# Optimization experiments

Hardware: AMD Instinct MI355X
Metric: run time of the kernel (lower is better)

The kernel has to match this reference:

```python
import jax, jax.numpy as jnp
import numpy as np

ENC_DIM = 128
DEC_DIM = 128
NUM_HEADS = 4
HEAD_DIM = DEC_DIM // NUM_HEADS


def _layernorm(x, g, b, eps=1e-5):
    mu = jnp.mean(x, axis=-1, keepdims=True)
    var = jnp.mean((x - mu) ** 2, axis=-1, keepdims=True)
    return (x - mu) * jax.lax.rsqrt(var + eps) * g + b


def setup_inputs() -> dict:
    key = jax.random.key(0)
    ks = jax.random.split(key, 12)
    B, H, W, D = 2, 16, 16, 16
    s = 0.02
    return {
        "encoder_feat": jax.random.normal(ks[0], (B, ENC_DIM, H, W, D), jnp.float32),
        "decoder_feat": jax.random.normal(ks[1], (B, DEC_DIM, H, W, D), jnp.float32),
        # torch Linear weights stored as [out, in]
        "Wq": jax.random.normal(ks[2], (DEC_DIM, DEC_DIM), jnp.float32) * s,
        "bq": jnp.zeros((DEC_DIM,), jnp.float32),
        "Wk": jax.random.normal(ks[3], (DEC_DIM, ENC_DIM), jnp.float32) * s,
        "bk": jnp.zeros((DEC_DIM,), jnp.float32),
        "Wv": jax.random.normal(ks[4], (DEC_DIM, ENC_DIM), jnp.float32) * s,
        "bv": jnp.zeros((DEC_DIM,), jnp.float32),
        "Wo": jax.random.normal(ks[5], (DEC_DIM, DEC_DIM), jnp.float32) * s,
        "bo": jnp.zeros((DEC_DIM,), jnp.float32),
        "g_enc": jnp.ones((ENC_DIM,), jnp.float32),
        "b_enc": jnp.zeros((ENC_DIM,), jnp.float32),
        "g_dec": jnp.ones((DEC_DIM,), jnp.float32),
        "b_dec": jnp.zeros((DEC_DIM,), jnp.float32),
        "g_out": jnp.ones((DEC_DIM,), jnp.float32),
        "b_out": jnp.zeros((DEC_DIM,), jnp.float32),
        "W1": jax.random.normal(ks[6], (DEC_DIM * 4, DEC_DIM), jnp.float32) * s,
        "b1": jnp.zeros((DEC_DIM * 4,), jnp.float32),
        "W2": jax.random.normal(ks[7], (DEC_DIM, DEC_DIM * 4), jnp.float32) * s,
        "b2": jnp.zeros((DEC_DIM,), jnp.float32),
    }


def reference(encoder_feat, decoder_feat, Wq, bq, Wk, bk, Wv, bv, Wo, bo,
              g_enc, b_enc, g_dec, b_dec, g_out, b_out, W1, b1, W2, b2):
    B, C_dec, H, W_, D = decoder_feat.shape
    N = H * W_ * D
    scale = HEAD_DIM ** -0.5
    # [B, C, H, W, D] -> [B, N, C]
    enc_seq = encoder_feat.reshape(B, -1, N).transpose(0, 2, 1)
    dec_seq = decoder_feat.reshape(B, C_dec, N).transpose(0, 2, 1)
    enc_seq = _layernorm(enc_seq, g_enc, b_enc)
    dec_seq = _layernorm(dec_seq, g_dec, b_dec)
    # projections (torch Linear: x @ W.T + b), split heads -> [B, h, N, d]
    Q = (dec_seq @ Wq.T + bq).reshape(B, N, NUM_HEADS, HEAD_DIM).transpose(0, 2, 1, 3)
    K = (enc_seq @ Wk.T + bk).reshape(B, N, NUM_HEADS, HEAD_DIM).transpose(0, 2, 1, 3)
    V = (enc_seq @ Wv.T + bv).reshape(B, N, NUM_HEADS, HEAD_DIM).transpose(0, 2, 1, 3)
    attn = jnp.einsum('bhqd,bhkd->bhqk', Q, K) * scale  # [B, h, N, N]
    attn = jax.nn.softmax(attn, axis=-1)
    out = jnp.einsum('bhqk,bhkd->bhqd', attn, V)
    out = out.transpose(0, 2, 1, 3).reshape(B, N, C_dec)
    out = out @ Wo.T + bo
    out = dec_seq + out
    h = _layernorm(out, g_out, b_out)
    ffn = jax.nn.gelu(h @ W1.T + b1, approximate=False) @ W2.T + b2
    out = out + ffn
    return out.transpose(0, 2, 1).reshape(B, C_dec, H, W_, D)
```

## Files before the change

### kernel.cpp

```cpp
#include <hip/hip_runtime.h>
#include <hip/hip_bf16.h>
#include <math.h>

#define B_ 2
#define N_ 4096
#define BN_ 8192
#define NH_ 4
#define SPLIT_ 8

using bf16x8   = __attribute__((ext_vector_type(8))) __bf16;
using f32x4    = __attribute__((ext_vector_type(4))) float;
using ushortx8 = __attribute__((ext_vector_type(8))) unsigned short;

#if __has_builtin(__builtin_amdgcn_exp2f)
#define FAST_EXP2(x) __builtin_amdgcn_exp2f(x)
#else
#define FAST_EXP2(x) __expf((x) * 0.6931471805599453f)
#endif

static __device__ __forceinline__ unsigned short f2bf(float f) {
    union { __hip_bfloat16 h; unsigned short u; } c;
    c.h = __float2bfloat16(f);
    return c.u;
}
static __device__ __forceinline__ float bf2f(unsigned short u) {
    union { __hip_bfloat16 h; unsigned short u; } c;
    c.u = u;
    return __bfloat162float(c.h);
}
static __device__ __forceinline__ unsigned int pk2bf(float lo, float hi) {
    return __builtin_amdgcn_perm(__float_as_uint(hi) + 0x8000u,
                                 __float_as_uint(lo) + 0x8000u, 0x07060302u);
}

__global__ __launch_bounds__(256)
void fused_pre_kernel(const float* __restrict__ Wq, const float* __restrict__ Wk,
                      const float* __restrict__ Wv, const float* __restrict__ Wo,
                      const float* __restrict__ W1, const float* __restrict__ W2,
                      unsigned short* __restrict__ wq, unsigned short* __restrict__ wk,
                      unsigned short* __restrict__ wv, unsigned short* __restrict__ wo,
                      unsigned short* __restrict__ w1, unsigned short* __restrict__ w2,
                      const float* __restrict__ enc, const float* __restrict__ dec,
                      const float* __restrict__ g_enc, const float* __restrict__ b_enc,
                      const float* __restrict__ g_dec, const float* __restrict__ b_dec,
                      unsigned short* __restrict__ enc_out,
                      unsigned short* __restrict__ dec_out) {
    __shared__ float tile[128][33];
    __shared__ float mu_s[32], inv_s[32];
    const int t = threadIdx.x;
    if (blockIdx.x < 768) {
        const int id = blockIdx.x * 256 + t;
        if      (id <  16384) wq[id]          = f2bf(Wq[id]);
        else if (id <  32768) wk[id - 16384]  = f2bf(Wk[id - 16384]);
        else if (id <  49152) wv[id - 32768]  = f2bf(Wv[id - 32768]);
        else if (id <  65536) wo[id - 49152]  = f2bf(Wo[id - 49152]);
        else if (id < 131072) w1[id - 65536]  = f2bf(W1[id - 65536]);
        else                  w2[id - 131072] = f2bf(W2[id - 131072]);
        return;
    }
    const int idx = blockIdx.x - 768;
    const int x = idx & 127;
    const int b = (idx >> 7) & 1;
    const int z = idx >> 8;
    const float* in     = z ? dec   : enc;
    const float* gamma  = z ? g_dec : g_enc;
    const float* beta   = z ? b_dec : b_enc;
    unsigned short* outb = z ? dec_out : enc_out;
    const int n0 = x * 32;
    const float* inb = in + (size_t)b * 128 * N_;

    {
        const int col = t & 31;
        const int r0  = t >> 5;
        for (int j = 0; j < 16; ++j) {
            const int r = r0 + 8 * j;
            tile[r][col] = inb[(size_t)r * N_ + n0 + col];
        }
    }
    __syncthreads();
    {
        const int tok = t >> 3;
        const int ln  = t & 7;
        float s = 0.f, ss = 0.f;
        for (int c = ln; c < 128; c += 8) {
            const float x2 = tile[c][tok];
            s += x2; ss += x2 * x2;
        }
        for (int m = 1; m < 8; m <<= 1) {
            s  += __shfl_xor(s, m);
            ss += __shfl_xor(ss, m);
        }
        if (ln == 0) {
            const float mu  = s * (1.f / 128.f);
            const float var = ss * (1.f / 128.f) - mu * mu;
            mu_s[tok]  = mu;
            inv_s[tok] = rsqrtf(var + 1e-5f);
        }
    }
    __syncthreads();
    const size_t obase = ((size_t)b * N_ + n0) * 128;
    for (int j = 0; j < 16; ++j) {
        const int f  = t + 256 * j;
        const int tk = f >> 7;
        const int c  = f & 127;
        const float x2 = tile[c][tk];
        outb[obase + f] = f2bf((x2 - mu_s[tk]) * inv_s[tk] * gamma[c] + beta[c]);
    }
}

__global__ __launch_bounds__(128)
void qkv_gemm_kernel(const unsigned short* __restrict__ decb,
                     const unsigned short* __restrict__ encb,
                     const unsigned short* __restrict__ wq,
                     const unsigned short* __restrict__ wk,
                     const unsigned short* __restrict__ wv,
                     const float* __restrict__ bq, const float* __restrict__ bk,
                     const float* __restrict__ bv,
                     unsigned short* __restrict__ Qh, unsigned short* __restrict__ Kh,
                     unsigned short* __restrict__ Vt) {
    const int z = blockIdx.y;
    const int t = threadIdx.x;
    const int wvx = t >> 6, lane = t & 63;
    const int l15 = lane & 15, quad = lane >> 4;
    const int m0 = blockIdx.x * 32 + wvx * 16;
    const unsigned short* X    = (z == 0) ? decb : encb;
    const unsigned short* Wb   = (z == 0) ? wq : (z == 1) ? wk : wv;
    const float*          bias = (z == 0) ? bq : (z == 1) ? bk : bv;

    bf16x8 af[4];
    #pragma unroll
    for (int kk = 0; kk < 4; ++kk)
        af[kk] = *(const bf16x8*)(X + (size_t)(m0 + l15) * 128 + kk * 32 + quad * 8);

    f32x4 acc[8];
    #pragma unroll
    for (int nb = 0; nb < 8; ++nb) {
        f32x4 a = {0.f, 0.f, 0.f, 0.f};
        #pragma unroll
        for (int kk = 0; kk < 4; ++kk) {
            const bf16x8 wf = *(const bf16x8*)(Wb + (size_t)(nb * 16 + l15) * 128 + kk * 32 + quad * 8);
            a = __builtin_amdgcn_mfma_f32_16x16x32_bf16(af[kk], wf, a, 0, 0, 0);
        }
        acc[nb] = a;
    }

    const float qsc = 0.17677669529663687f * 1.4426950408889634f;
    const int b   = m0 >> 12;
    const int nb0 = (m0 & 4095) + quad * 4;
    #pragma unroll
    for (int nb = 0; nb < 8; ++nb) {
        const int col = nb * 16 + l15;
        const int h = col >> 5, d = col & 31;
        const float bz = bias[col];
        if (z == 2) {
            ushort4 pk;
            pk.x = f2bf(acc[nb][0] + bz);
            pk.y = f2bf(acc[nb][1] + bz);
            pk.z = f2bf(acc[nb][2] + bz);
            pk.w = f2bf(acc[nb][3] + bz);
            *(ushort4*)(Vt + ((size_t)(b * NH_ + h) * 32 + d) * N_ + nb0) = pk;
        } else {
            unsigned short* dst = (z == 0) ? Qh : Kh;
            const float sc = (z == 0) ? qsc : 1.f;
            #pragma unroll
            for (int r = 0; r < 4; ++r) {
                const int n = nb0 + r;
                dst[((size_t)(b * NH_ + h) * N_ + n) * 32 + d] = f2bf((acc[nb][r] + bz) * sc);
            }
        }
    }
}

__global__ __launch_bounds__(256)
void attn_kernel5(const unsigned short* __restrict__ Qh,
                  const unsigned short* __restrict__ Kh,
                  const unsigned short* __restrict__ Vt,
                  unsigned short* __restrict__ Op,
                  unsigned short* __restrict__ lp) {
    __shared__ alignas(16) unsigned short sP[4][64][72];

    const int gid   = blockIdx.x;
    const int combo = gid & 63;
    const int qblk  = gid >> 6;
    const int bh    = combo & 7;
    const int s     = combo >> 3;
    const int t  = threadIdx.x;
    const int wvx = t >> 6, lane = t & 63;
    const int l15 = lane & 15, quad = lane >> 4;
    const int qw = qblk * 256 + wvx * 64;
    const size_t hbse = (size_t)bh * N_ * 32;

    bf16x8 qf[4];
    #pragma unroll
    for (int f = 0; f < 4; ++f)
        qf[f] = *(const bf16x8*)(Qh + hbse + (size_t)(qw + f * 16 + l15) * 32 + quad * 8);

    const unsigned short* Kp = Kh + hbse;
    const unsigned short* Vp = Vt + (size_t)bh * 32 * N_;

    f32x4 o0[4], o1[4];
    float l[4];
    #pragma unroll
    for (int f = 0; f < 4; ++f) {
        o0[f] = f32x4{0.f, 0.f, 0.f, 0.f};
        o1[f] = f32x4{0.f, 0.f, 0.f, 0.f};
        l[f] = 0.f;
    }
    const f32x4 zero = {0.f, 0.f, 0.f, 0.f};

    const int kbeg = s * (N_ / SPLIT_);
    const int kend = kbeg + (N_ / SPLIT_);

    bf16x8 kf[4];
    #pragma unroll
    for (int c = 0; c < 4; ++c)
        kf[c] = *(const bf16x8*)(Kp + (size_t)(kbeg + c * 16 + l15) * 32 + quad * 8);

    for (int k0 = kbeg; k0 < kend; k0 += 64) {
        bf16x8 va[2], vb[2];
        #pragma unroll
        for (int s2 = 0; s2 < 2; ++s2) {
            va[s2] = *(const bf16x8*)(Vp + (size_t)l15 * N_        + k0 + s2 * 32 + quad * 8);
            vb[s2] = *(const bf16x8*)(Vp + (size_t)(16 + l15) * N_ + k0 + s2 * 32 + quad * 8);
        }
        const int kn = (k0 + 64 < kend) ? (k0 + 64) : kbeg;
        bf16x8 kfn[4];
        #pragma unroll
        for (int c = 0; c < 4; ++c)
            kfn[c] = *(const bf16x8*)(Kp + (size_t)(kn + c * 16 + l15) * 32 + quad * 8);

        #pragma unroll
        for (int f = 0; f < 4; ++f) {
            #pragma unroll
            for (int c = 0; c < 4; ++c) {
                const f32x4 sv = __builtin_amdgcn_mfma_f32_16x16x32_bf16(kf[c], qf[f], zero, 0, 0, 0);
                const float p0 = FAST_EXP2(sv[0]);
                const float p1 = FAST_EXP2(sv[1]);
                const float p2 = FAST_EXP2(sv[2]);
                const float p3 = FAST_EXP2(sv[3]);
                l[f] += (p0 + p1) + (p2 + p3);
                uint2 pk;
                pk.x = pk2bf(p0, p1);
                pk.y = pk2bf(p2, p3);
                *(uint2*)&sP[wvx][f * 16 + l15][c * 16 + quad * 4] = pk;
            }
        }
        #pragma unroll
        for (int f = 0; f < 4; ++f) {
            #pragma unroll
            for (int s2 = 0; s2 < 2; ++s2) {
                const bf16x8 pf = *(const bf16x8*)&sP[wvx][f * 16 + l15][s2 * 32 + quad * 8];
                o0[f] = __builtin_amdgcn_mfma_f32_16x16x32_bf16(va[s2], pf, o0[f], 0, 0, 0);
                o1[f] = __builtin_amdgcn_mfma_f32_16x16x32_bf16(vb[s2], pf, o1[f], 0, 0, 0);
            }
        }
        #pragma unroll
        for (int c = 0; c < 4; ++c) kf[c] = kfn[c];
    }

    #pragma unroll
    for (int f = 0; f < 4; ++f) {
        float lf = l[f];
        lf += __shfl_xor(lf, 16);
        lf += __shfl_xor(lf, 32);
        const int tok = qw + f * 16 + l15;
        const size_t ob = ((size_t)(s * 8 + bh) * N_ + tok) * 32;
        uint2 w0, w1v;
        w0.x  = pk2bf(o0[f][0], o0[f][1]); w0.y  = pk2bf(o0[f][2], o0[f][3]);
        w1v.x = pk2bf(o1[f][0], o1[f][1]); w1v.y = pk2bf(o1[f][2], o1[f][3]);
        *(uint2*)&Op[ob + quad * 4]      = w0;
        *(uint2*)&Op[ob + 16 + quad * 4] = w1v;
        if (quad == 0)
            lp[(size_t)(s * 8 + bh) * N_ + tok] = f2bf(lf);
    }
}

__global__ __launch_bounds__(256)
void fused_tail2_kernel(const unsigned short* __restrict__ Op,
                        const unsigned short* __restrict__ lp,
                        const unsigned short* __restrict__ wo,
                        const float* __restrict__ bo,
                        const unsigned short* __restrict__ decb,
                        const float* __restrict__ g, const float* __restrict__ be,
                        const unsigned short* __restrict__ w1,
                        const float* __restrict__ b1,
                        const unsigned short* __restrict__ w2,
                        const float* __restrict__ b2,
                        float* __restrict__ out) {
    __shared__ alignas(16) float sred[4][64][32];
    __shared__ float sln[4][2][16];
    __shared__ alignas(16) unsigned short hb_lds[16][136];
    __shared__ alignas(16) unsigned short smid[16][536];
    const int t = threadIdx.x;
    const int wv = t >> 6, lane = t & 63;
    const int l15 = lane & 15, quad = lane >> 4;
    const int m0 = blockIdx.x * 16;

    const int tokA = m0 + l15;
    const int bA = tokA >> 12, nA = tokA & 4095;
    const int bhh = bA * NH_ + wv;
    bf16x8 af;
    {
        f32x4 sa = {0.f, 0.f, 0.f, 0.f}, sb = {0.f, 0.f, 0.f, 0.f};
        float lt = 0.f;
        #pragma unroll
        for (int s = 0; s < SPLIT_; ++s) {
            const size_t base = ((size_t)(s * 8 + bhh) * N_ + nA) * 32 + quad * 8;
            const ushortx8 u = *(const ushortx8*)&Op[base];
            sa[0] += bf2f(u[0]); sa[1] += bf2f(u[1]);
            sa[2] += bf2f(u[2]); sa[3] += bf2f(u[3]);
            sb[0] += bf2f(u[4]); sb[1] += bf2f(u[5]);
            sb[2] += bf2f(u[6]); sb[3] += bf2f(u[7]);
            lt += bf2f(lp[(size_t)(s * 8 + bhh) * N_ + nA]);
        }
        const float inv = 1.f / lt;
        union { uint4 u; bf16x8 v; } cvt;
        cvt.u.x = pk2bf(sa[0] * inv, sa[1] * inv);
        cvt.u.y = pk2bf(sa[2] * inv, sa[3] * inv);
        cvt.u.z = pk2bf(sb[0] * inv, sb[1] * inv);
        cvt.u.w = pk2bf(sb[2] * inv, sb[3] * inv);
        af = cvt.v;
    }

    #pragma unroll
    for (int nb = 0; nb < 8; ++nb) {
        const bf16x8 wf = *(const bf16x8*)(wo + (size_t)(nb * 16 + l15) * 128
                                           + wv * 32 + quad * 8);
        const f32x4 a = __builtin_amdgcn_mfma_f32_16x16x32_bf16(
            af, wf, f32x4{0.f, 0.f, 0.f, 0.f}, 0, 0, 0);
        *(f32x4*)&sred[wv][lane][nb * 4] = a;
    }
    __syncthreads();

    float v[2][4];
    #pragma unroll
    for (int lnb = 0; lnb < 2; ++lnb) {
        const int nbg = 2 * wv + lnb;
        f32x4 p = *(const f32x4*)&sred[0][lane][nbg * 4];
        p += *(const f32x4*)&sred[1][lane][nbg * 4];
        p += *(const f32x4*)&sred[2][lane][nbg * 4];
        p += *(const f32x4*)&sred[3][lane][nbg * 4];
        const int col = nbg * 16 + l15;
        const float bz = bo[col];
        #pragma unroll
        for (int r = 0; r < 4; ++r) {
            const int tok = m0 + quad * 4 + r;
            v[lnb][r] = p[r] + bz + bf2f(decb[(size_t)tok * 128 + col]);
        }
    }

    {
        float s[4], ss[4];
        #pragma unroll
        for (int r = 0; r < 4; ++r) {
            float a = v[0][r] + v[1][r];
            float b = v[0][r] * v[0][r] + v[1][r] * v[1][r];
            for (int m = 1; m < 16; m <<= 1) {
                a += __shfl_xor(a, m);
                b += __shfl_xor(b, m);
            }
            s[r] = a; ss[r] = b;
        }
        if (l15 == 0) {
            #pragma unroll
            for (int r = 0; r < 4; ++r) {
                sln[wv][0][quad * 4 + r] = s[r];
                sln[wv][1][quad * 4 + r] = ss[r];
            }
        }
    }
    __syncthreads();

    {
        #pragma unroll
        for (int r = 0; r < 4; ++r) {
            const int tk = quad * 4 + r;
            const float stot  = sln[0][0][tk] + sln[1][0][tk] + sln[2][0][tk] + sln[3][0][tk];
            const float sstot = sln[0][1][tk] + sln[1][1][tk] + sln[2][1][tk] + sln[3][1][tk];
            const float mu  = stot * (1.f / 128.f);
            const float inv = rsqrtf(sstot * (1.f / 128.f) - mu * mu + 1e-5f);
            #pragma unroll
            for (int lnb = 0; lnb < 2; ++lnb) {
                const int col = (2 * wv + lnb) * 16 + l15;
                hb_lds[tk][col] = f2bf((v[lnb][r] - mu) * inv * g[col] + be[col]);
            }
        }
    }
    __syncthreads();

    bf16x8 hf[4];
    #pragma unroll
    for (int kk = 0; kk < 4; ++kk)
        hf[kk] = *(const bf16x8*)&hb_lds[l15][kk * 32 + quad * 8];
    #pragma unroll
    for (int nb = 0; nb < 8; ++nb) {
        const int col = wv * 128 + nb * 16 + l15;
        f32x4 a = {0.f, 0.f, 0.f, 0.f};
        #pragma unroll
        for (int kk = 0; kk < 4; ++kk) {
            const bf16x8 wf = *(const bf16x8*)(w1 + (size_t)col * 128 + kk * 32 + quad * 8);
            a = __builtin_amdgcn_mfma_f32_16x16x32_bf16(hf[kk], wf, a, 0, 0, 0);
        }
        const float bz = b1[col];
        #pragma unroll
        for (int r = 0; r < 4; ++r) {
            float x = a[r] + bz;
            x = 0.5f * x * (1.f + erff(x * 0.70710678118f));
            smid[quad * 4 + r][col] = f2bf(x);
        }
    }
    __syncthreads();

    f32x4 acc[8];
    #pragma unroll
    for (int nb = 0; nb < 8; ++nb) acc[nb] = f32x4{0.f, 0.f, 0.f, 0.f};
    #pragma unroll
    for (int kk = 0; kk < 4; ++kk) {
        const bf16x8 af2 = *(const bf16x8*)&smid[l15][wv * 128 + kk * 32 + quad * 8];
        #pragma unroll
        for (int nb = 0; nb < 8; ++nb) {
            const bf16x8 wf = *(const bf16x8*)(w2 + (size_t)(nb * 16 + l15) * 512
                                               + wv * 128 + kk * 32 + quad * 8);
            acc[nb] = __builtin_amdgcn_mfma_f32_16x16x32_bf16(af2, wf, acc[nb], 0, 0, 0);
        }
    }
    #pragma unroll
    for (int nb = 0; nb < 8; ++nb)
        *(f32x4*)&sred[wv][lane][nb * 4] = acc[nb];
    __syncthreads();

    {
        const int b = m0 >> 12;
        const int nb0 = (m0 & 4095) + quad * 4;
        #pragma unroll
        for (int lnb = 0; lnb < 2; ++lnb) {
            const int nbg = 2 * wv + lnb;
            f32x4 p = *(const f32x4*)&sred[0][lane][nbg * 4];
            p += *(const f32x4*)&sred[1][lane][nbg * 4];
            p += *(const f32x4*)&sred[2][lane][nbg * 4];
            p += *(const f32x4*)&sred[3][lane][nbg * 4];
            const int col = nbg * 16 + l15;
            const float bz = b2[col];
            f32x4 res;
            #pragma unroll
            for (int r = 0; r < 4; ++r)
                res[r] = p[r] + bz + v[lnb][r];
            *(f32x4*)&out[((size_t)(b * 128 + col)) * N_ + nb0] = res;
        }
    }
}

extern "C" void kernel_launch(void* const* d_in, const int* in_sizes, int n_in,
                              void* d_out, int out_size, void* d_ws, size_t ws_size,
                              hipStream_t stream) {
    const float* enc   = (const float*)d_in[0];
    const float* dec   = (const float*)d_in[1];
    const float* Wq    = (const float*)d_in[2];
    const float* bq    = (const float*)d_in[3];
    const float* Wk    = (const float*)d_in[4];
    const float* bk    = (const float*)d_in[5];
    const float* Wv    = (const float*)d_in[6];
    const float* bv    = (const float*)d_in[7];
    const float* Wo    = (const float*)d_in[8];
    const float* bo    = (const float*)d_in[9];
    const float* g_enc = (const float*)d_in[10];
    const float* b_enc = (const float*)d_in[11];
    const float* g_dec = (const float*)d_in[12];
    const float* b_dec = (const float*)d_in[13];
    const float* g_out = (const float*)d_in[14];
    const float* b_out = (const float*)d_in[15];
    const float* W1    = (const float*)d_in[16];
    const float* b1    = (const float*)d_in[17];
    const float* W2    = (const float*)d_in[18];
    const float* b2    = (const float*)d_in[19];
    float* out = (float*)d_out;
    char*  W   = (char*)d_ws;

    unsigned short* wqb = (unsigned short*)(W);
    unsigned short* wkb = wqb + 16384;
    unsigned short* wvb = wkb + 16384;
    unsigned short* wob = wvb + 16384;
    unsigned short* w1b = wob + 16384;
    unsigned short* w2b = w1b + 65536;
    unsigned short* enc_lnb = (unsigned short*)(W + (512ull  << 10));
    unsigned short* dec_lnb = (unsigned short*)(W + (2560ull << 10));
    unsigned short* Qh      = (unsigned short*)(W + (4608ull << 10));
    unsigned short* Kh      = (unsigned short*)(W + (6656ull << 10));
    unsigned short* Vt      = (unsigned short*)(W + (8704ull << 10));
    unsigned short* Op      = (unsigned short*)(W + (10752ull << 10));
    unsigned short* lpb     = (unsigned short*)(W + (27136ull << 10));

    fused_pre_kernel<<<1280, 256, 0, stream>>>(
        Wq, Wk, Wv, Wo, W1, W2, wqb, wkb, wvb, wob, w1b, w2b,
        enc, dec, g_enc, b_enc, g_dec, b_dec, enc_lnb, dec_lnb);

    qkv_gemm_kernel<<<dim3(BN_ / 32, 3), 128, 0, stream>>>(
        dec_lnb, enc_lnb, wqb, wkb, wvb, bq, bk, bv, Qh, Kh, Vt);

    attn_kernel5<<<1024, 256, 0, stream>>>(Qh, Kh, Vt, Op, lpb);

    fused_tail2_kernel<<<512, 256, 0, stream>>>(Op, lpb, wob, bo, dec_lnb,
                                                g_out, b_out, w1b, b1, w2b, b2, out);
}
```

Measured before the change: 174.7 us.

## Fuse input LayerNorm into QKV projection and split output columns across blocks

Moves the encoder/decoder LayerNorm out of the pre-kernel and into the QKV GEMM. Each wave now reads the fp32 channel-major inputs directly, computes mean and variance with cross-lane shuffles, and feeds normalized bf16 fragments to MFMA. This removes the bf16 LN intermediate round-trip, though the decoder LN is still written out for the tail kernel. The grid gains a z-dimension that splits the 128 output columns into two halves, which adds parallelism but makes every half recompute the LN and re-read the encoder data. The weight conversion becomes its own small kernel.

```diff
diff --git a/kernel.cpp b/kernel.cpp
--- a/kernel.cpp
+++ b/kernel.cpp
@@ -34,139 +34,105 @@
 }
 
 __global__ __launch_bounds__(256)
-void fused_pre_kernel(const float* __restrict__ Wq, const float* __restrict__ Wk,
-                      const float* __restrict__ Wv, const float* __restrict__ Wo,
-                      const float* __restrict__ W1, const float* __restrict__ W2,
-                      unsigned short* __restrict__ wq, unsigned short* __restrict__ wk,
-                      unsigned short* __restrict__ wv, unsigned short* __restrict__ wo,
-                      unsigned short* __restrict__ w1, unsigned short* __restrict__ w2,
-                      const float* __restrict__ enc, const float* __restrict__ dec,
-                      const float* __restrict__ g_enc, const float* __restrict__ b_enc,
-                      const float* __restrict__ g_dec, const float* __restrict__ b_dec,
-                      unsigned short* __restrict__ enc_out,
-                      unsigned short* __restrict__ dec_out) {
-    __shared__ float tile[128][33];
-    __shared__ float mu_s[32], inv_s[32];
-    const int t = threadIdx.x;
-    if (blockIdx.x < 768) {
-        const int id = blockIdx.x * 256 + t;
-        if      (id <  16384) wq[id]          = f2bf(Wq[id]);
-        else if (id <  32768) wk[id - 16384]  = f2bf(Wk[id - 16384]);
-        else if (id <  49152) wv[id - 32768]  = f2bf(Wv[id - 32768]);
-        else if (id <  65536) wo[id - 49152]  = f2bf(Wo[id - 49152]);
-        else if (id < 131072) w1[id - 65536]  = f2bf(W1[id - 65536]);
-        else                  w2[id - 131072] = f2bf(W2[id - 131072]);
-        return;
-    }
-    const int idx = blockIdx.x - 768;
-    const int x = idx & 127;
-    const int b = (idx >> 7) & 1;
-    const int z = idx >> 8;
-    const float* in     = z ? dec   : enc;
-    const float* gamma  = z ? g_dec : g_enc;
-    const float* beta   = z ? b_dec : b_enc;
-    unsigned short* outb = z ? dec_out : enc_out;
-    const int n0 = x * 32;
-    const float* inb = in + (size_t)b * 128 * N_;
-
-    {
-        const int col = t & 31;
-        const int r0  = t >> 5;
-        for (int j = 0; j < 16; ++j) {
-            const int r = r0 + 8 * j;
-            tile[r][col] = inb[(size_t)r * N_ + n0 + col];
-        }
-    }
-    __syncthreads();
-    {
-        const int tok = t >> 3;
-        const int ln  = t & 7;
-        float s = 0.f, ss = 0.f;
-        for (int c = ln; c < 128; c += 8) {
-            const float x2 = tile[c][tok];
-            s += x2; ss += x2 * x2;
-        }
-        for (int m = 1; m < 8; m <<= 1) {
-            s  += __shfl_xor(s, m);
-            ss += __shfl_xor(ss, m);
-        }
-        if (ln == 0) {
-            const float mu  = s * (1.f / 128.f);
-            const float var = ss * (1.f / 128.f) - mu * mu;
-            mu_s[tok]  = mu;
-            inv_s[tok] = rsqrtf(var + 1e-5f);
-        }
-    }
-    __syncthreads();
-    const size_t obase = ((size_t)b * N_ + n0) * 128;
-    for (int j = 0; j < 16; ++j) {
-        const int f  = t + 256 * j;
-        const int tk = f >> 7;
-        const int c  = f & 127;
-        const float x2 = tile[c][tk];
-        outb[obase + f] = f2bf((x2 - mu_s[tk]) * inv_s[tk] * gamma[c] + beta[c]);
-    }
+void convert_weights_kernel(const float* __restrict__ Wq, const float* __restrict__ Wk,
+                            const float* __restrict__ Wv, const float* __restrict__ Wo,
+                            const float* __restrict__ W1, const float* __restrict__ W2,
+                            unsigned short* __restrict__ wq, unsigned short* __restrict__ wk,
+                            unsigned short* __restrict__ wv, unsigned short* __restrict__ wo,
+                            unsigned short* __restrict__ w1, unsigned short* __restrict__ w2) {
+    const int id = blockIdx.x * 256 + threadIdx.x;
+    if      (id <  16384) wq[id]          = f2bf(Wq[id]);
+    else if (id <  32768) wk[id - 16384]  = f2bf(Wk[id - 16384]);
+    else if (id <  49152) wv[id - 32768]  = f2bf(Wv[id - 32768]);
+    else if (id <  65536) wo[id - 49152]  = f2bf(Wo[id - 49152]);
+    else if (id < 131072) w1[id - 65536]  = f2bf(W1[id - 65536]);
+    else                  w2[id - 131072] = f2bf(W2[id - 131072]);
 }
 
 __global__ __launch_bounds__(128)
-void qkv_gemm_kernel(const unsigned short* __restrict__ decb,
-                     const unsigned short* __restrict__ encb,
-                     const unsigned short* __restrict__ wq,
-                     const unsigned short* __restrict__ wk,
-                     const unsigned short* __restrict__ wv,
-                     const float* __restrict__ bq, const float* __restrict__ bk,
-                     const float* __restrict__ bv,
-                     unsigned short* __restrict__ Qh, unsigned short* __restrict__ Kh,
-                     unsigned short* __restrict__ Vt) {
-    const int z = blockIdx.y;
+void qkv_ln_kernel(const float* __restrict__ enc, const float* __restrict__ dec,
+                   const float* __restrict__ g_enc, const float* __restrict__ b_enc,
+                   const float* __restrict__ g_dec, const float* __restrict__ b_dec,
+                   const unsigned short* __restrict__ wq,
+                   const unsigned short* __restrict__ wk,
+                   const unsigned short* __restrict__ wv,
+                   const float* __restrict__ bq, const float* __restrict__ bk,
+                   const float* __restrict__ bv,
+                   unsigned short* __restrict__ Qh, unsigned short* __restrict__ Kh,
+                   unsigned short* __restrict__ Vt,
+                   unsigned short* __restrict__ dec_lnb) {
+    const int z    = blockIdx.y;
+    const int half = blockIdx.z;
     const int t = threadIdx.x;
     const int wvx = t >> 6, lane = t & 63;
     const int l15 = lane & 15, quad = lane >> 4;
     const int m0 = blockIdx.x * 32 + wvx * 16;
-    const unsigned short* X    = (z == 0) ? decb : encb;
-    const unsigned short* Wb   = (z == 0) ? wq : (z == 1) ? wk : wv;
-    const float*          bias = (z == 0) ? bq : (z == 1) ? bk : bv;
+    const int b = m0 >> 12, n0 = m0 & 4095;
+    const float* inb   = ((z == 0) ? dec : enc) + (size_t)b * 128 * N_;
+    const float* gamma = (z == 0) ? g_dec : g_enc;
+    const float* beta  = (z == 0) ? b_dec : b_enc;
+    const unsigned short* Wb = (z == 0) ? wq : (z == 1) ? wk : wv;
+    const float* bias        = (z == 0) ? bq : (z == 1) ? bk : bv;
+
+    float x[4][8];
+    float s = 0.f, ss = 0.f;
+    #pragma unroll
+    for (int kk = 0; kk < 4; ++kk) {
+        #pragma unroll
+        for (int j = 0; j < 8; ++j) {
+            const int c = kk * 32 + quad * 8 + j;
+            const float v = inb[(size_t)c * N_ + n0 + l15];
+            x[kk][j] = v; s += v; ss += v * v;
+        }
+    }
+    s  += __shfl_xor(s, 16);  s  += __shfl_xor(s, 32);
+    ss += __shfl_xor(ss, 16); ss += __shfl_xor(ss, 32);
+    const float mu  = s * (1.f / 128.f);
+    const float inv = rsqrtf(ss * (1.f / 128.f) - mu * mu + 1e-5f);
 
     bf16x8 af[4];
     #pragma unroll
-    for (int kk = 0; kk < 4; ++kk)
-        af[kk] = *(const bf16x8*)(X + (size_t)(m0 + l15) * 128 + kk * 32 + quad * 8);
-
-    f32x4 acc[8];
-    #pragma unroll
-    for (int nb = 0; nb < 8; ++nb) {
+    for (int kk = 0; kk < 4; ++kk) {
+        float y[8];
+        #pragma unroll
+        for (int j = 0; j < 8; ++j) {
+            const int c = kk * 32 + quad * 8 + j;
+            y[j] = (x[kk][j] - mu) * inv * gamma[c] + beta[c];
+        }
+        union { uint4 u; bf16x8 v8; ushortx8 us; } cvt;
+        cvt.u.x = pk2bf(y[0], y[1]); cvt.u.y = pk2bf(y[2], y[3]);
+        cvt.u.z = pk2bf(y[4], y[5]); cvt.u.w = pk2bf(y[6], y[7]);
+        af[kk] = cvt.v8;
+        if (z == 0 && half == 0)
+            *(ushortx8*)(dec_lnb + (size_t)(m0 + l15) * 128 + kk * 32 + quad * 8) = cvt.us;
+    }
+
+    const float qsc = 0.17677669529663687f * 1.4426950408889634f;
+    const int nb0 = n0 + quad * 4;
+    #pragma unroll
+    for (int nb = 0; nb < 4; ++nb) {
+        const int col = half * 64 + nb * 16 + l15;
         f32x4 a = {0.f, 0.f, 0.f, 0.f};
         #pragma unroll
         for (int kk = 0; kk < 4; ++kk) {
-            const bf16x8 wf = *(const bf16x8*)(Wb + (size_t)(nb * 16 + l15) * 128 + kk * 32 + quad * 8);
+            const bf16x8 wf = *(const bf16x8*)(Wb + (size_t)col * 128 + kk * 32 + quad * 8);
             a = __builtin_amdgcn_mfma_f32_16x16x32_bf16(af[kk], wf, a, 0, 0, 0);
         }
-        acc[nb] = a;
-    }
-
-    const float qsc = 0.17677669529663687f * 1.4426950408889634f;
-    const int b   = m0 >> 12;
-    const int nb0 = (m0 & 4095) + quad * 4;
-    #pragma unroll
-    for (int nb = 0; nb < 8; ++nb) {
-        const int col = nb * 16 + l15;
         const int h = col >> 5, d = col & 31;
         const float bz = bias[col];
         if (z == 2) {
             ushort4 pk;
-            pk.x = f2bf(acc[nb][0] + bz);
-            pk.y = f2bf(acc[nb][1] + bz);
-            pk.z = f2bf(acc[nb][2] + bz);
-            pk.w = f2bf(acc[nb][3] + bz);
+            pk.x = f2bf(a[0] + bz);
+            pk.y = f2bf(a[1] + bz);
+            pk.z = f2bf(a[2] + bz);
+            pk.w = f2bf(a[3] + bz);
             *(ushort4*)(Vt + ((size_t)(b * NH_ + h) * 32 + d) * N_ + nb0) = pk;
         } else {
             unsigned short* dst = (z == 0) ? Qh : Kh;
             const float sc = (z == 0) ? qsc : 1.f;
             #pragma unroll
-            for (int r = 0; r < 4; ++r) {
-                const int n = nb0 + r;
-                dst[((size_t)(b * NH_ + h) * N_ + n) * 32 + d] = f2bf((acc[nb][r] + bz) * sc);
-            }
+            for (int r = 0; r < 4; ++r)
+                dst[((size_t)(b * NH_ + h) * N_ + nb0 + r) * 32 + d] = f2bf((a[r] + bz) * sc);
         }
     }
 }
@@ -482,7 +448,6 @@
     unsigned short* wob = wvb + 16384;
     unsigned short* w1b = wob + 16384;
     unsigned short* w2b = w1b + 65536;
-    unsigned short* enc_lnb = (unsigned short*)(W + (512ull  << 10));
     unsigned short* dec_lnb = (unsigned short*)(W + (2560ull << 10));
     unsigned short* Qh      = (unsigned short*)(W + (4608ull << 10));
     unsigned short* Kh      = (unsigned short*)(W + (6656ull << 10));
@@ -490,12 +455,12 @@
     unsigned short* Op      = (unsigned short*)(W + (10752ull << 10));
     unsigned short* lpb     = (unsigned short*)(W + (27136ull << 10));
 
-    fused_pre_kernel<<<1280, 256, 0, stream>>>(
-        Wq, Wk, Wv, Wo, W1, W2, wqb, wkb, wvb, wob, w1b, w2b,
-        enc, dec, g_enc, b_enc, g_dec, b_dec, enc_lnb, dec_lnb);
-
-    qkv_gemm_kernel<<<dim3(BN_ / 32, 3), 128, 0, stream>>>(
-        dec_lnb, enc_lnb, wqb, wkb, wvb, bq, bk, bv, Qh, Kh, Vt);
+    convert_weights_kernel<<<768, 256, 0, stream>>>(Wq, Wk, Wv, Wo, W1, W2,
+                                                    wqb, wkb, wvb, wob, w1b, w2b);
+
+    qkv_ln_kernel<<<dim3(BN_ / 32, 3, 2), 128, 0, stream>>>(
+        enc, dec, g_enc, b_enc, g_dec, b_dec, wqb, wkb, wvb,
+        bq, bk, bv, Qh, Kh, Vt, dec_lnb);
 
     attn_kernel5<<<1024, 256, 0, stream>>>(Qh, Kh, Vt, Op, lpb);
 
```

New measurement: 172.5 us. No clear change (-1.3%).
